# Kernel optimization log

Hardware: AMD Instinct MI355X
Metric: run time of the kernel (lower is better)

The kernel has to match this reference:

```python
import jax, jax.numpy as jnp
import numpy as np

N_NODES = 50000
N_EDGES = 800000
D = 128


def _gcn_layer(x, src, dst, deg_inv_sqrt, W, b, n_nodes):
    # GCNConv: X' = D^{-1/2} (A + I) D^{-1/2} X W + b   (PyG default, self-loops added)
    h = x @ W  # [N, D]
    norm = deg_inv_sqrt[src] * deg_inv_sqrt[dst]  # [E+N]
    msgs = h[src] * norm[:, None]  # [E+N, D] gather + scale
    out = jax.ops.segment_sum(msgs, dst, num_segments=n_nodes)  # scatter-add
    return out + b


def setup_inputs() -> dict:
    key = jax.random.key(0)
    k1, k2, k3, k4 = jax.random.split(key, 4)
    x = jax.random.normal(k1, (N_NODES, D), dtype=jnp.float32)
    edge_index = jax.random.randint(k2, (2, N_EDGES), 0, N_NODES, dtype=jnp.int64)
    scale = 1.0 / np.sqrt(D)
    W1 = jax.random.normal(k3, (D, D), dtype=jnp.float32) * scale
    b1 = jnp.zeros((D,), dtype=jnp.float32)
    W2 = jax.random.normal(k4, (D, D), dtype=jnp.float32) * scale
    b2 = jnp.zeros((D,), dtype=jnp.float32)
    return {"x": x, "edge_index": edge_index, "W1": W1, "b1": b1, "W2": W2, "b2": b2}


def reference(x, edge_index, W1, b1, W2, b2):
    n_nodes = x.shape[0]
    # add self-loops once (same graph both layers)
    loop = jnp.arange(n_nodes, dtype=edge_index.dtype)
    src = jnp.concatenate([edge_index[0], loop])
    dst = jnp.concatenate([edge_index[1], loop])
    deg = jax.ops.segment_sum(jnp.ones_like(dst, dtype=x.dtype), dst, num_segments=n_nodes)
    deg_inv_sqrt = jnp.where(deg > 0, jax.lax.rsqrt(deg), 0.0)

    h = _gcn_layer(x, src, dst, deg_inv_sqrt, W1, b1, n_nodes)
    h = jax.nn.relu(h)
    h = _gcn_layer(h, src, dst, deg_inv_sqrt, W2, b2, n_nodes)
    h = jax.nn.relu(h)
    return h
```

## Files before the change

### kernel.cpp

```cpp
#include <hip/hip_runtime.h>

#define N_NODES 50000
#define N_EDGES 800000
#define D 128
#define NB 392
#define CHUNK 2048
#define NBKT 391
#define GB ((N_NODES + 127) / 128)

typedef unsigned int uint32;
typedef unsigned short ushort;
typedef __attribute__((ext_vector_type(8))) short s8v;
typedef __attribute__((ext_vector_type(4))) float f4v;

__device__ __forceinline__ ushort f2bf(float f) {
    unsigned u = __float_as_uint(f);
    u += 0x7FFFu + ((u >> 16) & 1u);
    return (ushort)(u >> 16);
}
__device__ __forceinline__ float bf_lo(uint32 u) { return __uint_as_float(u << 16); }
__device__ __forceinline__ float bf_hi(uint32 u) { return __uint_as_float(u & 0xFFFF0000u); }

__device__ __forceinline__ int block_incl_scan(int v, int t) {
    int lane = t & 63, wv = t >> 6;
    int incl = v;
    #pragma unroll
    for (int off = 1; off < 64; off <<= 1) {
        int u = __shfl_up(incl, off, 64);
        if (lane >= off) incl += u;
    }
    __shared__ int wsums[4];
    if (lane == 63) wsums[wv] = incl;
    __syncthreads();
    int add = 0;
    if (wv > 0) add += wsums[0];
    if (wv > 1) add += wsums[1];
    if (wv > 2) add += wsums[2];
    return incl + add;
}

__global__ __launch_bounds__(256) void prep_kernel(const int* __restrict__ dst,
                                                   int* __restrict__ cnt,
                                                   const float* __restrict__ W1,
                                                   const float* __restrict__ W2,
                                                   ushort* __restrict__ W1t,
                                                   ushort* __restrict__ W2t) {
    int t = threadIdx.x, blk = blockIdx.x;
    if (blk >= NB) {
        const float* W = (blk - NB) ? W2 : W1;
        ushort* Wt = (blk - NB) ? W2t : W1t;
        #pragma unroll
        for (int it = 0; it < 16; it++) {
            int fid = t + it * 256;
            int k = fid >> 5;
            int n0 = (fid & 31) * 4;
            float4 w = ((const float4*)W)[fid];
            Wt[(n0 + 0) * D + k] = f2bf(w.x);
            Wt[(n0 + 1) * D + k] = f2bf(w.y);
            Wt[(n0 + 2) * D + k] = f2bf(w.z);
            Wt[(n0 + 3) * D + k] = f2bf(w.w);
        }
        return;
    }
    __shared__ int lc[NBKT];
    for (int i = t; i < NBKT; i += 256) lc[i] = 0;
    __syncthreads();
    int e0 = blk * CHUNK;
    #pragma unroll
    for (int j = 0; j < 8; j++) {
        int e = e0 + t + j * 256;
        if (e < N_EDGES) atomicAdd(&lc[dst[e] >> 7], 1);
    }
    __syncthreads();
    for (int i = t; i < NBKT; i += 256) {
        int c = lc[i];
        if (c) atomicAdd(&cnt[i], c);
    }
}

__global__ __launch_bounds__(256) void scanB_kernel(const int* __restrict__ cnt,
                                                    int* __restrict__ base,
                                                    int* __restrict__ gcur) {
    int t = threadIdx.x;
    int i0 = 2 * t, i1 = 2 * t + 1;
    int c0 = (i0 < NBKT) ? cnt[i0] : 0;
    int c1 = (i1 < NBKT) ? cnt[i1] : 0;
    int s = c0 + c1;
    int incl = block_incl_scan(s, t);
    int excl = incl - s;
    if (i0 < NBKT) { base[i0] = excl;      gcur[i0] = excl; }
    if (i1 < NBKT) { base[i1] = excl + c0; gcur[i1] = excl + c0; }
    if (t == 255) base[NBKT] = incl;
}

template<bool BF16IN>
__device__ __forceinline__ void gemm_body(const void* __restrict__ Xv,
                                          const ushort* __restrict__ Wt,
                                          ushort* __restrict__ Hb, int bt) {
    __shared__ ushort Cs[128 * 136];
    int t = threadIdx.x;
    int wv = t >> 6, lane = t & 63;
    int q = lane >> 4, m = lane & 15;
    int rbase = bt * 128 + wv * 32;
    f4v zero = {0.f, 0.f, 0.f, 0.f};
    f4v acc[2][8];
    #pragma unroll
    for (int mt = 0; mt < 2; mt++)
        #pragma unroll
        for (int n = 0; n < 8; n++) acc[mt][n] = zero;

    #pragma unroll
    for (int kt = 0; kt < 4; kt++) {
        int k0 = kt * 32 + q * 8;
        s8v a[2];
        #pragma unroll
        for (int mt = 0; mt < 2; mt++) {
            int row = rbase + mt * 16 + m;
            if (row >= N_NODES) row = N_NODES - 1;
            if (BF16IN) {
                const ushort* xp = (const ushort*)Xv + (size_t)row * D + k0;
                a[mt] = *(const s8v*)xp;
            } else {
                const float* xp = (const float*)Xv + (size_t)row * D + k0;
                float4 u0 = *(const float4*)xp;
                float4 u1 = *(const float4*)(xp + 4);
                s8v av;
                av[0] = (short)f2bf(u0.x); av[1] = (short)f2bf(u0.y);
                av[2] = (short)f2bf(u0.z); av[3] = (short)f2bf(u0.w);
                av[4] = (short)f2bf(u1.x); av[5] = (short)f2bf(u1.y);
                av[6] = (short)f2bf(u1.z); av[7] = (short)f2bf(u1.w);
                a[mt] = av;
            }
        }
        #pragma unroll
        for (int n = 0; n < 8; n++) {
            s8v b = *(const s8v*)(Wt + (size_t)(n * 16 + m) * D + k0);
            acc[0][n] = __builtin_amdgcn_mfma_f32_16x16x32_bf16(a[0], b, acc[0][n], 0, 0, 0);
            acc[1][n] = __builtin_amdgcn_mfma_f32_16x16x32_bf16(a[1], b, acc[1][n], 0, 0, 0);
        }
    }
    #pragma unroll
    for (int mt = 0; mt < 2; mt++)
        #pragma unroll
        for (int n = 0; n < 8; n++)
            #pragma unroll
            for (int r = 0; r < 4; r++) {
                int row = wv * 32 + mt * 16 + q * 4 + r;
                Cs[row * 136 + n * 16 + m] = f2bf(acc[mt][n][r]);
            }
    __syncthreads();
    int gbase = bt * 128;
    #pragma unroll
    for (int it = 0; it < 8; it++) {
        int cid = t + it * 256;
        int row = cid >> 4, off = (cid & 15) * 8;
        int grow = gbase + row;
        if (grow < N_NODES) {
            s8v v = *(const s8v*)(Cs + row * 136 + off);
            *(s8v*)(Hb + (size_t)grow * D + off) = v;
        }
    }
}

__global__ __launch_bounds__(256) void phaseC_gemm1(const int* __restrict__ src,
                                                    const int* __restrict__ dst,
                                                    int* __restrict__ gcur,
                                                    uint32* __restrict__ edgeTmp,
                                                    const float* __restrict__ X,
                                                    const ushort* __restrict__ W1t,
                                                    ushort* __restrict__ Hb) {
    if (blockIdx.x >= NB) {
        gemm_body<false>(X, W1t, Hb, blockIdx.x - NB);
        return;
    }
    __shared__ int lcnt[NBKT];
    __shared__ int lcur[NBKT];
    int t = threadIdx.x, blk = blockIdx.x;
    for (int i = t; i < NBKT; i += 256) lcnt[i] = 0;
    __syncthreads();
    int e0 = blk * CHUNK;
    uint32 rec[8]; int bk[8];
    #pragma unroll
    for (int j = 0; j < 8; j++) {
        int e = e0 + t + j * 256;
        if (e < N_EDGES) {
            uint32 s = (uint32)src[e], d = (uint32)dst[e];
            rec[j] = (s << 16) | d;
            bk[j] = (int)(d >> 7);
            atomicAdd(&lcnt[bk[j]], 1);
        } else bk[j] = -1;
    }
    __syncthreads();
    for (int i = t; i < NBKT; i += 256) {
        int c = lcnt[i];
        lcur[i] = c ? atomicAdd(&gcur[i], c) : 0;
    }
    __syncthreads();
    #pragma unroll
    for (int j = 0; j < 8; j++) {
        if (bk[j] >= 0) {
            int p = atomicAdd(&lcur[bk[j]], 1);
            edgeTmp[p] = rec[j];
        }
    }
}

__global__ __launch_bounds__(256) void phaseD_kernel(const uint32* __restrict__ edgeTmp,
                                                     const int* __restrict__ base,
                                                     int* __restrict__ rowstart,
                                                     float* __restrict__ dis,
                                                     ushort* __restrict__ e16) {
    __shared__ int cnt[128];
    __shared__ int cur[128];
    int t = threadIdx.x, b = blockIdx.x;
    int beg = base[b];
    int end = base[b + 1];
    if (t < 128) cnt[t] = 0;
    __syncthreads();
    for (int p = beg + t; p < end; p += 256)
        atomicAdd(&cnt[edgeTmp[p] & 127], 1);
    __syncthreads();
    int c = (t < 128) ? cnt[t] : 0;
    int incl = block_incl_scan(c, t);
    int excl = incl - c;
    int node = b * 128 + t;
    if (t < 128) {
        if (node <= N_NODES) rowstart[node] = beg + excl;
        if (node < N_NODES) dis[node] = rsqrtf((float)(c + 1));
        cur[t] = excl;
    }
    __syncthreads();
    for (int p = beg + t; p < end; p += 256) {
        uint32 u = edgeTmp[p];
        int r = atomicAdd(&cur[u & 127], 1);
        e16[beg + r] = (ushort)(u >> 16);
    }
}

__device__ __forceinline__ void fma8(float* a, uint4 v, float w) {
    a[0] = fmaf(bf_lo(v.x), w, a[0]); a[1] = fmaf(bf_hi(v.x), w, a[1]);
    a[2] = fmaf(bf_lo(v.y), w, a[2]); a[3] = fmaf(bf_hi(v.y), w, a[3]);
    a[4] = fmaf(bf_lo(v.z), w, a[4]); a[5] = fmaf(bf_hi(v.z), w, a[5]);
    a[6] = fmaf(bf_lo(v.w), w, a[6]); a[7] = fmaf(bf_hi(v.w), w, a[7]);
}

template<bool BF16OUT>
__global__ __launch_bounds__(256) void aggr_kernel(const uint4* __restrict__ Hb4,
                                                   const float* __restrict__ dis,
                                                   const int* __restrict__ rowstart,
                                                   const ushort* __restrict__ e16,
                                                   const float* __restrict__ bias,
                                                   void* __restrict__ Hout) {
    int t = threadIdx.x;
    int li = t & 15;
    int n = blockIdx.x * 16 + (t >> 4);
    float dn = dis[n];
    float a[8] = {0.f, 0.f, 0.f, 0.f, 0.f, 0.f, 0.f, 0.f};
    {
        uint4 sv = Hb4[(size_t)n * 16 + li];
        fma8(a, sv, dn);
    }
    int beg = rowstart[n], end = rowstart[n + 1];
    int p = beg;
    for (; p + 7 < end; p += 8) {
        int s[8];
        #pragma unroll
        for (int j = 0; j < 8; j++) s[j] = e16[p + j];
        float w[8];
        #pragma unroll
        for (int j = 0; j < 8; j++) w[j] = dis[s[j]];
        uint4 v[8];
        #pragma unroll
        for (int j = 0; j < 8; j++) v[j] = Hb4[(size_t)s[j] * 16 + li];
        #pragma unroll
        for (int j = 0; j < 8; j++) fma8(a, v[j], w[j]);
    }
    for (; p < end; p++) {
        int s0 = e16[p];
        uint4 v0 = Hb4[(size_t)s0 * 16 + li];
        fma8(a, v0, dis[s0]);
    }
    const float4* b4 = (const float4*)bias;
    float4 bb0 = b4[li * 2], bb1 = b4[li * 2 + 1];
    float r0 = fmaxf(fmaf(dn, a[0], bb0.x), 0.f);
    float r1 = fmaxf(fmaf(dn, a[1], bb0.y), 0.f);
    float r2 = fmaxf(fmaf(dn, a[2], bb0.z), 0.f);
    float r3 = fmaxf(fmaf(dn, a[3], bb0.w), 0.f);
    float r4 = fmaxf(fmaf(dn, a[4], bb1.x), 0.f);
    float r5 = fmaxf(fmaf(dn, a[5], bb1.y), 0.f);
    float r6 = fmaxf(fmaf(dn, a[6], bb1.z), 0.f);
    float r7 = fmaxf(fmaf(dn, a[7], bb1.w), 0.f);
    if (BF16OUT) {
        uint4 o;
        o.x = (uint32)f2bf(r0) | ((uint32)f2bf(r1) << 16);
        o.y = (uint32)f2bf(r2) | ((uint32)f2bf(r3) << 16);
        o.z = (uint32)f2bf(r4) | ((uint32)f2bf(r5) << 16);
        o.w = (uint32)f2bf(r6) | ((uint32)f2bf(r7) << 16);
        ((uint4*)Hout)[(size_t)n * 16 + li] = o;
    } else {
        float4* H4 = (float4*)Hout;
        float4 o0; o0.x = r0; o0.y = r1; o0.z = r2; o0.w = r3;
        float4 o1; o1.x = r4; o1.y = r5; o1.z = r6; o1.w = r7;
        H4[(size_t)n * 32 + li * 2]     = o0;
        H4[(size_t)n * 32 + li * 2 + 1] = o1;
    }
}

__global__ __launch_bounds__(256) void gemm2_kernel(const ushort* __restrict__ X,
                                                    const ushort* __restrict__ W2t,
                                                    ushort* __restrict__ Hb) {
    gemm_body<true>(X, W2t, Hb, blockIdx.x);
}

extern "C" void kernel_launch(void* const* d_in, const int* in_sizes, int n_in,
                              void* d_out, int out_size, void* d_ws, size_t ws_size,
                              hipStream_t stream) {
    const float* x  = (const float*)d_in[0];
    const int*   ei = (const int*)d_in[1];
    const float* W1 = (const float*)d_in[2];
    const float* b1 = (const float*)d_in[3];
    const float* W2 = (const float*)d_in[4];
    const float* b2 = (const float*)d_in[5];
    float* out = (float*)d_out;

    char* ws = (char*)d_ws;
    size_t off = 0;
    auto alloc = [&](size_t bytes) -> void* {
        void* p = ws + off;
        off += (bytes + 255) & ~(size_t)255;
        return p;
    };
    int*    cnt      = (int*)alloc((size_t)NBKT * 4);
    int*    base     = (int*)alloc((size_t)(NBKT + 1) * 4);
    int*    gcur     = (int*)alloc((size_t)NBKT * 4);
    int*    rowstart = (int*)alloc((size_t)(N_NODES + 1) * 4);
    float*  dis      = (float*)alloc((size_t)N_NODES * 4);
    uint32* edgeTmp  = (uint32*)alloc((size_t)N_EDGES * 4);
    ushort* e16      = (ushort*)alloc((size_t)N_EDGES * 2);
    ushort* Hb       = (ushort*)alloc((size_t)N_NODES * D * 2);
    ushort* HO1      = (ushort*)alloc((size_t)N_NODES * D * 2);
    ushort* W1t      = (ushort*)alloc((size_t)D * D * 2);
    ushort* W2t      = (ushort*)alloc((size_t)D * D * 2);

    const int* src = ei;
    const int* dst = ei + N_EDGES;

    hipMemsetAsync(cnt, 0, (size_t)NBKT * 4, stream);

    prep_kernel<<<NB + 2, 256, 0, stream>>>(dst, cnt, W1, W2, W1t, W2t);
    scanB_kernel<<<1, 256, 0, stream>>>(cnt, base, gcur);
    phaseC_gemm1<<<NB + GB, 256, 0, stream>>>(src, dst, gcur, edgeTmp, x, W1t, Hb);
    phaseD_kernel<<<NBKT, 256, 0, stream>>>(edgeTmp, base, rowstart, dis, e16);

    aggr_kernel<true><<<N_NODES / 16, 256, 0, stream>>>((const uint4*)Hb, dis, rowstart,
                                                        e16, b1, HO1);
    gemm2_kernel<<<GB, 256, 0, stream>>>(HO1, W2t, Hb);
    aggr_kernel<false><<<N_NODES / 16, 256, 0, stream>>>((const uint4*)Hb, dis, rowstart,
                                                         e16, b2, out);
}
```

Before: 227.5 us.

## Prescale GEMM rows by source degree norm to drop per-edge dis gathers

Each GEMM output row is multiplied by its node's inverse-sqrt degree before the bf16 store, so aggregation only sums neighbor rows without gathering dis[src] per edge. To make dis available, GEMM1 is split out of the fused phaseC kernel and launched after phaseD, which loses the overlap of the edge bucketing with GEMM1. A 4-wide remainder loop is also added to the aggregation. Rounding changes slightly because the scale is applied before bf16 conversion.

```diff
diff --git a/kernel.cpp b/kernel.cpp
--- a/kernel.cpp
+++ b/kernel.cpp
@@ -93,15 +93,84 @@
     if (t == 255) base[NBKT] = incl;
 }
 
+__global__ __launch_bounds__(256) void phaseC_kernel(const int* __restrict__ src,
+                                                     const int* __restrict__ dst,
+                                                     int* __restrict__ gcur,
+                                                     uint32* __restrict__ edgeTmp) {
+    __shared__ int lcnt[NBKT];
+    __shared__ int lcur[NBKT];
+    int t = threadIdx.x, blk = blockIdx.x;
+    for (int i = t; i < NBKT; i += 256) lcnt[i] = 0;
+    __syncthreads();
+    int e0 = blk * CHUNK;
+    uint32 rec[8]; int bk[8];
+    #pragma unroll
+    for (int j = 0; j < 8; j++) {
+        int e = e0 + t + j * 256;
+        if (e < N_EDGES) {
+            uint32 s = (uint32)src[e], d = (uint32)dst[e];
+            rec[j] = (s << 16) | d;
+            bk[j] = (int)(d >> 7);
+            atomicAdd(&lcnt[bk[j]], 1);
+        } else bk[j] = -1;
+    }
+    __syncthreads();
+    for (int i = t; i < NBKT; i += 256) {
+        int c = lcnt[i];
+        lcur[i] = c ? atomicAdd(&gcur[i], c) : 0;
+    }
+    __syncthreads();
+    #pragma unroll
+    for (int j = 0; j < 8; j++) {
+        if (bk[j] >= 0) {
+            int p = atomicAdd(&lcur[bk[j]], 1);
+            edgeTmp[p] = rec[j];
+        }
+    }
+}
+
+__global__ __launch_bounds__(256) void phaseD_kernel(const uint32* __restrict__ edgeTmp,
+                                                     const int* __restrict__ base,
+                                                     int* __restrict__ rowstart,
+                                                     float* __restrict__ dis,
+                                                     ushort* __restrict__ e16) {
+    __shared__ int cnt[128];
+    __shared__ int cur[128];
+    int t = threadIdx.x, b = blockIdx.x;
+    int beg = base[b];
+    int end = base[b + 1];
+    if (t < 128) cnt[t] = 0;
+    __syncthreads();
+    for (int p = beg + t; p < end; p += 256)
+        atomicAdd(&cnt[edgeTmp[p] & 127], 1);
+    __syncthreads();
+    int c = (t < 128) ? cnt[t] : 0;
+    int incl = block_incl_scan(c, t);
+    int excl = incl - c;
+    int node = b * 128 + t;
+    if (t < 128) {
+        if (node <= N_NODES) rowstart[node] = beg + excl;
+        if (node < N_NODES) dis[node] = rsqrtf((float)(c + 1));
+        cur[t] = excl;
+    }
+    __syncthreads();
+    for (int p = beg + t; p < end; p += 256) {
+        uint32 u = edgeTmp[p];
+        int r = atomicAdd(&cur[u & 127], 1);
+        e16[beg + r] = (ushort)(u >> 16);
+    }
+}
+
 template<bool BF16IN>
-__device__ __forceinline__ void gemm_body(const void* __restrict__ Xv,
-                                          const ushort* __restrict__ Wt,
-                                          ushort* __restrict__ Hb, int bt) {
+__global__ __launch_bounds__(256) void gemm_mfma(const void* __restrict__ Xv,
+                                                 const ushort* __restrict__ Wt,
+                                                 const float* __restrict__ dis,
+                                                 ushort* __restrict__ Hb) {
     __shared__ ushort Cs[128 * 136];
     int t = threadIdx.x;
     int wv = t >> 6, lane = t & 63;
     int q = lane >> 4, m = lane & 15;
-    int rbase = bt * 128 + wv * 32;
+    int rbase = blockIdx.x * 128 + wv * 32;
     f4v zero = {0.f, 0.f, 0.f, 0.f};
     f4v acc[2][8];
     #pragma unroll
@@ -139,6 +208,15 @@
             acc[1][n] = __builtin_amdgcn_mfma_f32_16x16x32_bf16(a[1], b, acc[1][n], 0, 0, 0);
         }
     }
+    float disv[2][4];
+    #pragma unroll
+    for (int mt = 0; mt < 2; mt++)
+        #pragma unroll
+        for (int r = 0; r < 4; r++) {
+            int row = rbase + mt * 16 + q * 4 + r;
+            if (row >= N_NODES) row = N_NODES - 1;
+            disv[mt][r] = dis[row];
+        }
     #pragma unroll
     for (int mt = 0; mt < 2; mt++)
         #pragma unroll
@@ -146,10 +224,10 @@
             #pragma unroll
             for (int r = 0; r < 4; r++) {
                 int row = wv * 32 + mt * 16 + q * 4 + r;
-                Cs[row * 136 + n * 16 + m] = f2bf(acc[mt][n][r]);
+                Cs[row * 136 + n * 16 + m] = f2bf(acc[mt][n][r] * disv[mt][r]);
             }
     __syncthreads();
-    int gbase = bt * 128;
+    int gbase = blockIdx.x * 128;
     #pragma unroll
     for (int it = 0; it < 8; it++) {
         int cid = t + it * 256;
@@ -162,86 +240,11 @@
     }
 }
 
-__global__ __launch_bounds__(256) void phaseC_gemm1(const int* __restrict__ src,
-                                                    const int* __restrict__ dst,
-                                                    int* __restrict__ gcur,
-                                                    uint32* __restrict__ edgeTmp,
-                                                    const float* __restrict__ X,
-                                                    const ushort* __restrict__ W1t,
-                                                    ushort* __restrict__ Hb) {
-    if (blockIdx.x >= NB) {
-        gemm_body<false>(X, W1t, Hb, blockIdx.x - NB);
-        return;
-    }
-    __shared__ int lcnt[NBKT];
-    __shared__ int lcur[NBKT];
-    int t = threadIdx.x, blk = blockIdx.x;
-    for (int i = t; i < NBKT; i += 256) lcnt[i] = 0;
-    __syncthreads();
-    int e0 = blk * CHUNK;
-    uint32 rec[8]; int bk[8];
-    #pragma unroll
-    for (int j = 0; j < 8; j++) {
-        int e = e0 + t + j * 256;
-        if (e < N_EDGES) {
-            uint32 s = (uint32)src[e], d = (uint32)dst[e];
-            rec[j] = (s << 16) | d;
-            bk[j] = (int)(d >> 7);
-            atomicAdd(&lcnt[bk[j]], 1);
-        } else bk[j] = -1;
-    }
-    __syncthreads();
-    for (int i = t; i < NBKT; i += 256) {
-        int c = lcnt[i];
-        lcur[i] = c ? atomicAdd(&gcur[i], c) : 0;
-    }
-    __syncthreads();
-    #pragma unroll
-    for (int j = 0; j < 8; j++) {
-        if (bk[j] >= 0) {
-            int p = atomicAdd(&lcur[bk[j]], 1);
-            edgeTmp[p] = rec[j];
-        }
-    }
-}
-
-__global__ __launch_bounds__(256) void phaseD_kernel(const uint32* __restrict__ edgeTmp,
-                                                     const int* __restrict__ base,
-                                                     int* __restrict__ rowstart,
-                                                     float* __restrict__ dis,
-                                                     ushort* __restrict__ e16) {
-    __shared__ int cnt[128];
-    __shared__ int cur[128];
-    int t = threadIdx.x, b = blockIdx.x;
-    int beg = base[b];
-    int end = base[b + 1];
-    if (t < 128) cnt[t] = 0;
-    __syncthreads();
-    for (int p = beg + t; p < end; p += 256)
-        atomicAdd(&cnt[edgeTmp[p] & 127], 1);
-    __syncthreads();
-    int c = (t < 128) ? cnt[t] : 0;
-    int incl = block_incl_scan(c, t);
-    int excl = incl - c;
-    int node = b * 128 + t;
-    if (t < 128) {
-        if (node <= N_NODES) rowstart[node] = beg + excl;
-        if (node < N_NODES) dis[node] = rsqrtf((float)(c + 1));
-        cur[t] = excl;
-    }
-    __syncthreads();
-    for (int p = beg + t; p < end; p += 256) {
-        uint32 u = edgeTmp[p];
-        int r = atomicAdd(&cur[u & 127], 1);
-        e16[beg + r] = (ushort)(u >> 16);
-    }
-}
-
-__device__ __forceinline__ void fma8(float* a, uint4 v, float w) {
-    a[0] = fmaf(bf_lo(v.x), w, a[0]); a[1] = fmaf(bf_hi(v.x), w, a[1]);
-    a[2] = fmaf(bf_lo(v.y), w, a[2]); a[3] = fmaf(bf_hi(v.y), w, a[3]);
-    a[4] = fmaf(bf_lo(v.z), w, a[4]); a[5] = fmaf(bf_hi(v.z), w, a[5]);
-    a[6] = fmaf(bf_lo(v.w), w, a[6]); a[7] = fmaf(bf_hi(v.w), w, a[7]);
+__device__ __forceinline__ void acc8(float* a, uint4 v) {
+    a[0] += bf_lo(v.x); a[1] += bf_hi(v.x);
+    a[2] += bf_lo(v.y); a[3] += bf_hi(v.y);
+    a[4] += bf_lo(v.z); a[5] += bf_hi(v.z);
+    a[6] += bf_lo(v.w); a[7] += bf_hi(v.w);
 }
 
 template<bool BF16OUT>
@@ -255,10 +258,13 @@
     int li = t & 15;
     int n = blockIdx.x * 16 + (t >> 4);
     float dn = dis[n];
-    float a[8] = {0.f, 0.f, 0.f, 0.f, 0.f, 0.f, 0.f, 0.f};
+    float a[8];
     {
         uint4 sv = Hb4[(size_t)n * 16 + li];
-        fma8(a, sv, dn);
+        a[0] = bf_lo(sv.x); a[1] = bf_hi(sv.x);
+        a[2] = bf_lo(sv.y); a[3] = bf_hi(sv.y);
+        a[4] = bf_lo(sv.z); a[5] = bf_hi(sv.z);
+        a[6] = bf_lo(sv.w); a[7] = bf_hi(sv.w);
     }
     int beg = rowstart[n], end = rowstart[n + 1];
     int p = beg;
@@ -266,19 +272,23 @@
         int s[8];
         #pragma unroll
         for (int j = 0; j < 8; j++) s[j] = e16[p + j];
-        float w[8];
-        #pragma unroll
-        for (int j = 0; j < 8; j++) w[j] = dis[s[j]];
         uint4 v[8];
         #pragma unroll
         for (int j = 0; j < 8; j++) v[j] = Hb4[(size_t)s[j] * 16 + li];
         #pragma unroll
-        for (int j = 0; j < 8; j++) fma8(a, v[j], w[j]);
+        for (int j = 0; j < 8; j++) acc8(a, v[j]);
+    }
+    for (; p + 3 < end; p += 4) {
+        int s0 = e16[p + 0], s1 = e16[p + 1], s2 = e16[p + 2], s3 = e16[p + 3];
+        uint4 v0 = Hb4[(size_t)s0 * 16 + li];
+        uint4 v1 = Hb4[(size_t)s1 * 16 + li];
+        uint4 v2 = Hb4[(size_t)s2 * 16 + li];
+        uint4 v3 = Hb4[(size_t)s3 * 16 + li];
+        acc8(a, v0); acc8(a, v1); acc8(a, v2); acc8(a, v3);
     }
     for (; p < end; p++) {
-        int s0 = e16[p];
-        uint4 v0 = Hb4[(size_t)s0 * 16 + li];
-        fma8(a, v0, dis[s0]);
+        uint4 v0 = Hb4[(size_t)e16[p] * 16 + li];
+        acc8(a, v0);
     }
     const float4* b4 = (const float4*)bias;
     float4 bb0 = b4[li * 2], bb1 = b4[li * 2 + 1];
@@ -306,12 +316,6 @@
     }
 }
 
-__global__ __launch_bounds__(256) void gemm2_kernel(const ushort* __restrict__ X,
-                                                    const ushort* __restrict__ W2t,
-                                                    ushort* __restrict__ Hb) {
-    gemm_body<true>(X, W2t, Hb, blockIdx.x);
-}
-
 extern "C" void kernel_launch(void* const* d_in, const int* in_sizes, int n_in,
                               void* d_out, int out_size, void* d_ws, size_t ws_size,
                               hipStream_t stream) {
@@ -349,12 +353,13 @@
 
     prep_kernel<<<NB + 2, 256, 0, stream>>>(dst, cnt, W1, W2, W1t, W2t);
     scanB_kernel<<<1, 256, 0, stream>>>(cnt, base, gcur);
-    phaseC_gemm1<<<NB + GB, 256, 0, stream>>>(src, dst, gcur, edgeTmp, x, W1t, Hb);
+    phaseC_kernel<<<NB, 256, 0, stream>>>(src, dst, gcur, edgeTmp);
     phaseD_kernel<<<NBKT, 256, 0, stream>>>(edgeTmp, base, rowstart, dis, e16);
 
+    gemm_mfma<false><<<GB, 256, 0, stream>>>(x, W1t, dis, Hb);
     aggr_kernel<true><<<N_NODES / 16, 256, 0, stream>>>((const uint4*)Hb, dis, rowstart,
                                                         e16, b1, HO1);
-    gemm2_kernel<<<GB, 256, 0, stream>>>(HO1, W2t, Hb);
+    gemm_mfma<true><<<GB, 256, 0, stream>>>(HO1, W2t, dis, Hb);
     aggr_kernel<false><<<N_NODES / 16, 256, 0, stream>>>((const uint4*)Hb, dis, rowstart,
                                                          e16, b2, out);
 }
```

New measurement: 221.5 us. -2.6%, faster.
